# Optimization experiments

Hardware: AMD Instinct MI355X
Metric: run time of the kernel (lower is better)

## Reference

```python
import jax, jax.numpy as jnp
import numpy as np

N, E, F, NC, G = 50000, 400000, 128, 10, 64
EPS_BN = 1e-5
NEG_SLOPE = 0.2


def gat_conv(x, src, dst, W, a_src, a_dst, b, H, C):
    # PyG GATConv (concat=True): h = xW reshaped [N,H,C]; edge score =
    # leaky_relu(a_src.h_j + a_dst.h_i); softmax over incoming edges of i;
    # out_i = sum_j alpha_ij * h_j, then bias.
    n = x.shape[0]
    h = (x @ W).reshape(n, H, C)
    s_src = jnp.sum(h * a_src, axis=-1)  # [N,H]
    s_dst = jnp.sum(h * a_dst, axis=-1)  # [N,H]
    e = jax.nn.leaky_relu(s_src[src] + s_dst[dst], NEG_SLOPE)  # [E',H]
    m = jax.ops.segment_max(e, dst, num_segments=n)
    e = jnp.exp(e - m[dst])
    z = jax.ops.segment_sum(e, dst, num_segments=n)
    alpha = e / (z[dst] + 1e-16)
    msg = h[src] * alpha[:, :, None]  # [E',H,C]
    out = jax.ops.segment_sum(msg, dst, num_segments=n)
    return out.reshape(n, H * C) + b


def batch_norm(x, g, b):
    mu = jnp.mean(x, axis=0)
    var = jnp.var(x, axis=0)
    return g * (x - mu) * jax.lax.rsqrt(var + EPS_BN) + b


def setup_inputs() -> dict:
    key = jax.random.key(0)
    ks = jax.random.split(key, 32)
    d = {}
    d["x"] = jax.random.normal(ks[0], (N, F), dtype=jnp.float32)
    d["edge_index"] = jax.random.randint(ks[1], (2, E), 0, N, dtype=jnp.int32)
    d["batch"] = jnp.sort(jax.random.randint(ks[2], (N,), 0, G, dtype=jnp.int32))

    def nrm(k, shape, scale=0.1):
        return jax.random.normal(k, shape, dtype=jnp.float32) * scale

    # GATConv1: F -> 16, heads=20
    d["W1"] = nrm(ks[3], (F, 20 * 16))
    d["as1"] = nrm(ks[4], (20, 16))
    d["ad1"] = nrm(ks[5], (20, 16))
    d["b1"] = jnp.zeros((320,), jnp.float32)
    d["g1"], d["be1"] = jnp.ones((320,), jnp.float32), jnp.zeros((320,), jnp.float32)
    d["lw1"], d["lb1"] = nrm(ks[6], (320, 16)), jnp.zeros((16,), jnp.float32)
    d["gl1"], d["bel1"] = jnp.ones((16,), jnp.float32), jnp.zeros((16,), jnp.float32)
    # GATConv2: 16 -> 32, heads=16
    d["W2"] = nrm(ks[7], (16, 16 * 32))
    d["as2"] = nrm(ks[8], (16, 32))
    d["ad2"] = nrm(ks[9], (16, 32))
    d["b2"] = jnp.zeros((512,), jnp.float32)
    d["g2"], d["be2"] = jnp.ones((512,), jnp.float32), jnp.zeros((512,), jnp.float32)
    d["lw2"], d["lb2"] = nrm(ks[10], (512, 32)), jnp.zeros((32,), jnp.float32)
    d["gl2"], d["bel2"] = jnp.ones((32,), jnp.float32), jnp.zeros((32,), jnp.float32)
    # GATConv3: 32 -> 48, heads=8
    d["W3"] = nrm(ks[11], (32, 8 * 48))
    d["as3"] = nrm(ks[12], (8, 48))
    d["ad3"] = nrm(ks[13], (8, 48))
    d["b3"] = jnp.zeros((384,), jnp.float32)
    d["g3"], d["be3"] = jnp.ones((384,), jnp.float32), jnp.zeros((384,), jnp.float32)
    d["lwf"], d["lbf"] = nrm(ks[14], (384, NC)), jnp.zeros((NC,), jnp.float32)
    return d


def reference(x, edge_index, batch, W1, as1, ad1, b1, g1, be1, lw1, lb1, gl1, bel1,
              W2, as2, ad2, b2, g2, be2, lw2, lb2, gl2, bel2,
              W3, as3, ad3, b3, g3, be3, lwf, lbf):
    n = x.shape[0]
    loops = jnp.arange(n, dtype=edge_index.dtype)
    src = jnp.concatenate([edge_index[0], loops])
    dst = jnp.concatenate([edge_index[1], loops])

    h = gat_conv(x, src, dst, W1, as1, ad1, b1, 20, 16)
    h = jax.nn.relu(batch_norm(h, g1, be1))
    h = h @ lw1 + lb1
    h = jax.nn.relu(batch_norm(h, gl1, bel1))

    h = gat_conv(h, src, dst, W2, as2, ad2, b2, 16, 32)
    h = jax.nn.relu(batch_norm(h, g2, be2))
    h = h @ lw2 + lb2
    h = jax.nn.relu(batch_norm(h, gl2, bel2))

    h = gat_conv(h, src, dst, W3, as3, ad3, b3, 8, 48)
    h = jax.nn.relu(batch_norm(h, g3, be3))

    # global_mean_pool over graph ids
    sums = jax.ops.segment_sum(h, batch, num_segments=G)
    cnts = jax.ops.segment_sum(jnp.ones((n,), h.dtype), batch, num_segments=G)
    pooled = sums / jnp.maximum(cnts, 1.0)[:, None]
    # dropout is identity in eval mode
    return pooled @ lwf + lbf
```

## Files before the change

kernel.cpp:

```cpp
#include <hip/hip_runtime.h>
#include <cstdint>
#include <cstddef>

#define N_NODES 50000
#define N_EDGES 400000
#define TOT_E   450000
#define G_GRAPHS 64
#define PB 2048
#define SCAN_B 98

typedef unsigned short u16;
typedef unsigned int u32;
typedef unsigned char u8;
typedef __attribute__((ext_vector_type(8))) short s16x8;
typedef __attribute__((ext_vector_type(4))) float f32x4;
typedef __attribute__((ext_vector_type(2))) float f32x2;

__device__ __forceinline__ float b2f(u16 v) {
    union { u32 u; float f; } x; x.u = ((u32)v) << 16; return x.f;
}
__device__ __forceinline__ float lo2f(u32 u) {
    union { u32 u; float f; } x; x.u = u << 16; return x.f;
}
__device__ __forceinline__ float hi2f(u32 u) {
    union { u32 u; float f; } x; x.u = u & 0xffff0000u; return x.f;
}
__device__ __forceinline__ u16 f2b(float f) {
    union { float f; u32 u; } x; x.f = f;
    u32 r = x.u + 0x7fffu + ((x.u >> 16) & 1u);
    return (u16)(r >> 16);
}
__device__ __forceinline__ u32 pack2(float a, float b) {
    return (u32)f2b(a) | ((u32)f2b(b) << 16);
}

__global__ void k_init_deg(int* __restrict__ deg) {
    int i = blockIdx.x * blockDim.x + threadIdx.x;
    if (i < N_NODES) deg[i] = 1;
}

__global__ void k_hist(const int* __restrict__ ei, int* __restrict__ deg) {
    int e = blockIdx.x * blockDim.x + threadIdx.x;
    if (e < N_EDGES) atomicAdd(&deg[ei[N_EDGES + e]], 1);
}

__global__ void k_scan1(const int* __restrict__ deg, int* __restrict__ rowptr,
                        int* __restrict__ bsum) {
    __shared__ int buf[512];
    int tid = threadIdx.x;
    int i = blockIdx.x * 512 + tid;
    int v = (i < N_NODES) ? deg[i] : 0;
    buf[tid] = v;
    __syncthreads();
    for (int off = 1; off < 512; off <<= 1) {
        int t = (tid >= off) ? buf[tid - off] : 0;
        __syncthreads();
        buf[tid] += t;
        __syncthreads();
    }
    if (i < N_NODES) rowptr[i] = buf[tid] - v;
    if (tid == 511) bsum[blockIdx.x] = buf[511];
}

__global__ void k_scan2(int* __restrict__ bsum) {
    __shared__ int buf[128];
    int tid = threadIdx.x;
    int v = (tid < SCAN_B) ? bsum[tid] : 0;
    buf[tid] = v;
    __syncthreads();
    for (int off = 1; off < 128; off <<= 1) {
        int t = (tid >= off) ? buf[tid - off] : 0;
        __syncthreads();
        buf[tid] += t;
        __syncthreads();
    }
    if (tid < SCAN_B) bsum[tid] = buf[tid] - v;
}

__global__ void k_scan3(int* __restrict__ rowptr, int* __restrict__ cursor,
                        const int* __restrict__ bsum) {
    int i = blockIdx.x * blockDim.x + threadIdx.x;
    if (i < N_NODES) {
        int v = rowptr[i] + bsum[i >> 9];
        rowptr[i] = v;
        cursor[i] = v;
    }
    if (i == 0) rowptr[N_NODES] = TOT_E;
}

__global__ void k_scatter(const int* __restrict__ ei, int* __restrict__ cursor,
                          int* __restrict__ col, int* __restrict__ cdst) {
    int e = blockIdx.x * blockDim.x + threadIdx.x;
    if (e < N_EDGES) {
        int s = ei[e], d = ei[N_EDGES + e];
        int p = atomicAdd(&cursor[d], 1);
        col[p] = s;
        cdst[p] = d;
    } else if (e < TOT_E) {
        int i = e - N_EDGES;
        int p = atomicAdd(&cursor[i], 1);
        col[p] = i;
        cdst[p] = i;
    }
}

template<int K, int NO>
__global__ void k_wpack(const float* __restrict__ W, u16* __restrict__ Bp) {
    constexpr int KC = (K + 31) / 32;
    constexpr int NT = NO / 16;
    int idx = blockIdx.x * 256 + threadIdx.x;
    if (idx >= KC * NT * 64) return;
    int lane = idx & 63;
    int t = (idx >> 6) % NT;
    int c = (idx >> 6) / NT;
    int n = t * 16 + (lane & 15);
    int kbase = c * 32 + (lane >> 4) * 8;
    u16 v[8];
#pragma unroll
    for (int j = 0; j < 8; j++) {
        int k = kbase + j;
        v[j] = (k < K) ? f2b(W[(size_t)k * NO + n]) : (u16)0;
    }
    *(uint4*)(Bp + (size_t)idx * 8) = *(const uint4*)v;
}

template<int K, int NO, int H, int C>
__global__ void k_wtilde(const float* __restrict__ W, const float* __restrict__ as,
                         const float* __restrict__ ad, float* __restrict__ wts,
                         float* __restrict__ wtd) {
    static_assert((C % 4) == 0, "C divisible by 4");
    int t = threadIdx.x;
    if (t >= K * H) return;
    int k = t / H, h = t - k * H;
    float s1a = 0.f, s1b = 0.f, s1c = 0.f, s1d = 0.f;
    float s2a = 0.f, s2b = 0.f, s2c = 0.f, s2d = 0.f;
    const float* wr = W + (size_t)k * NO + h * C;
    const float* ar = as + h * C;
    const float* dr = ad + h * C;
    for (int c = 0; c < C; c += 4) {
        float w0 = wr[c], w1 = wr[c + 1], w2 = wr[c + 2], w3 = wr[c + 3];
        s1a = fmaf(w0, ar[c], s1a);     s1b = fmaf(w1, ar[c + 1], s1b);
        s1c = fmaf(w2, ar[c + 2], s1c); s1d = fmaf(w3, ar[c + 3], s1d);
        s2a = fmaf(w0, dr[c], s2a);     s2b = fmaf(w1, dr[c + 1], s2b);
        s2c = fmaf(w2, dr[c + 2], s2c); s2d = fmaf(w3, dr[c + 3], s2d);
    }
    wts[h * K + k] = (s1a + s1b) + (s1c + s1d);
    wtd[h * K + k] = (s2a + s2b) + (s2c + s2d);
}

template<int K>
__global__ void k_xform(const u16* __restrict__ X, const float* __restrict__ sc,
                        const float* __restrict__ sh, u16* __restrict__ Xt) {
    constexpr int NO2 = K / 2;
    int t = blockIdx.x * blockDim.x + threadIdx.x;
    if (t >= N_NODES * NO2) return;
    int w = t % NO2;
    u32 u = ((const u32*)X)[t];
    float2 scv = *(const float2*)&sc[2 * w];
    float2 shv = *(const float2*)&sh[2 * w];
    float a = fmaxf(lo2f(u) * scv.x + shv.x, 0.f);
    float b = fmaxf(hi2f(u) * scv.y + shv.y, 0.f);
    ((u32*)Xt)[t] = pack2(a, b);
}

template<int K, int H>
__global__ void k_scores_x(const u16* __restrict__ Xt, const float* __restrict__ wts,
                           const float* __restrict__ wtd, float* __restrict__ ssrc,
                           float* __restrict__ sdst) {
    int t = blockIdx.x * blockDim.x + threadIdx.x;
    if (t >= N_NODES * H) return;
    int i = t / H, h = t - i * H;
    const uint4* r = (const uint4*)(Xt + (size_t)i * K);
    const float4* ws = (const float4*)(wts + h * K);
    const float4* wd = (const float4*)(wtd + h * K);
    float s1 = 0.f, s2 = 0.f;
#pragma unroll
    for (int c8 = 0; c8 < K / 8; c8++) {
        uint4 u = r[c8];
        float v0 = lo2f(u.x), v1 = hi2f(u.x), v2 = lo2f(u.y), v3 = hi2f(u.y);
        float v4 = lo2f(u.z), v5 = hi2f(u.z), v6 = lo2f(u.w), v7 = hi2f(u.w);
        float4 aa = ws[c8 * 2], ab = ws[c8 * 2 + 1];
        float4 da = wd[c8 * 2], db = wd[c8 * 2 + 1];
        s1 = fmaf(v0, aa.x, fmaf(v1, aa.y, fmaf(v2, aa.z, fmaf(v3, aa.w, s1))));
        s1 = fmaf(v4, ab.x, fmaf(v5, ab.y, fmaf(v6, ab.z, fmaf(v7, ab.w, s1))));
        s2 = fmaf(v0, da.x, fmaf(v1, da.y, fmaf(v2, da.z, fmaf(v3, da.w, s2))));
        s2 = fmaf(v4, db.x, fmaf(v5, db.y, fmaf(v6, db.z, fmaf(v7, db.w, s2))));
    }
    ssrc[t] = s1;
    sdst[t] = s2;
}

template<int H, int K>
__global__ void k_aggx(const u16* __restrict__ Xt, const float* __restrict__ ssrc,
                       const float* __restrict__ sdst, const int* __restrict__ rowptr,
                       const int* __restrict__ col, u16* __restrict__ M) {
    constexpr int WPR = K / 2;
    constexpr int EPR = 64 / WPR;
    constexpr int Q = K / 4;
    static_assert(H * K == 256, "m row must be 256 elems (4/lane)");
    int wid = (int)((blockIdx.x * blockDim.x + threadIdx.x) >> 6);
    int lane = threadIdx.x & 63;
    if (wid >= N_NODES) return;
    int hl = lane / Q;
    int q = lane % Q;
    int lslot = lane / WPR;
    int lword = lane % WPR;
    float sd = (lane < H) ? sdst[(size_t)wid * H + lane] : 0.f;
    f32x2 acc01 = {0.f, 0.f}, acc23 = {0.f, 0.f};
    float z = 0.f;
    int beg = rowptr[wid], end = rowptr[wid + 1];
    for (int base = beg; base < end; base += 64) {
        int nmax = min(64, end - base);
        int myc = (base + lane < end) ? col[base + lane] : 0;
        int j = 0;
        for (; j + EPR <= nmax; j += EPR) {
            int ce = __shfl(myc, j + lslot);
            u32 g = *(const u32*)(Xt + (size_t)ce * K + lword * 2);
            int se[EPR];
#pragma unroll
            for (int e = 0; e < EPR; e++) se[e] = __shfl(myc, j + e);
            float w[EPR];
#pragma unroll
            for (int e = 0; e < EPR; e++) w[e] = 0.f;
            if (lane < H) {
#pragma unroll
                for (int e = 0; e < EPR; e++) {
                    float v = ssrc[(size_t)se[e] * H + lane] + sd;
                    v = (v > 0.f) ? v : 0.2f * v;
                    w[e] = __expf(v);
                    z += w[e];
                }
            }
#pragma unroll
            for (int e = 0; e < EPR; e++) {
                float al = __shfl(w[e], hl);
                u32 xa = __shfl(g, e * WPR + 2 * q);
                u32 xb = __shfl(g, e * WPR + 2 * q + 1);
                f32x2 al2 = {al, al};
                f32x2 xa2 = {lo2f(xa), hi2f(xa)};
                f32x2 xb2 = {lo2f(xb), hi2f(xb)};
                acc01 += xa2 * al2;
                acc23 += xb2 * al2;
            }
        }
        for (; j < nmax; j++) {
            int se = __shfl(myc, j);
            u32 g = *(const u32*)(Xt + (size_t)se * K + lword * 2);
            float w0 = 0.f;
            if (lane < H) {
                float v = ssrc[(size_t)se * H + lane] + sd;
                v = (v > 0.f) ? v : 0.2f * v;
                w0 = __expf(v);
                z += w0;
            }
            float al = __shfl(w0, hl);
            u32 xa = __shfl(g, 2 * q);
            u32 xb = __shfl(g, 2 * q + 1);
            f32x2 al2 = {al, al};
            f32x2 xa2 = {lo2f(xa), hi2f(xa)};
            f32x2 xb2 = {lo2f(xb), hi2f(xb)};
            acc01 += xa2 * al2;
            acc23 += xb2 * al2;
        }
    }
    float zk = __shfl(z, hl);
    float inv = 1.0f / (zk + 1e-16f);
    uint2 o;
    o.x = pack2(acc01.x * inv, acc01.y * inv);
    o.y = pack2(acc23.x * inv, acc23.y * inv);
    u32* orow = (u32*)(M + (size_t)wid * (H * K));
    *(uint2*)&orow[hl * WPR + 2 * q] = o;
}

template<int K, int NO, int C>
__global__ __launch_bounds__(256, 2)
void k_gemmd(const u16* __restrict__ M, const u16* __restrict__ Bp,
             const float* __restrict__ wb, u16* __restrict__ Y,
             float* __restrict__ pst) {
    constexpr int NT = NO / 16;
    constexpr int HK = (NO / C) * K;
    __shared__ float ls[2 * NO];
    int tid = threadIdx.x;
    for (int i = tid; i < 2 * NO; i += 256) ls[i] = 0.f;
    __syncthreads();
    int lane = threadIdx.x & 63;
    int wv = __builtin_amdgcn_readfirstlane((int)(threadIdx.x >> 6));
    int rbase = blockIdx.x * 64 + wv * 16;
    int m = lane & 15, quad = lane >> 4;
    int arow = rbase + m;
    if (arow >= N_NODES) arow = N_NODES - 1;
    const u16* xr = M + (size_t)arow * HK;
#pragma unroll
    for (int t = 0; t < NT; t++) {
        int h = (t * 16) / C;
        s16x8 a;
        if (K == 32 || quad < 2) {
            a = *(const s16x8*)(xr + h * K + quad * 8);
        } else {
#pragma unroll
            for (int j = 0; j < 8; j++) a[j] = 0;
        }
        s16x8 b = *(const s16x8*)(Bp + ((size_t)(t * 64 + lane)) * 8);
        f32x4 acc = (f32x4){0.f, 0.f, 0.f, 0.f};
        acc = __builtin_amdgcn_mfma_f32_16x16x32_bf16(a, b, acc, 0, 0, 0);
        int colb = t * 16 + m;
        float bv = wb[colb];
        float s = 0.f, q = 0.f;
#pragma unroll
        for (int i = 0; i < 4; i++) {
            int grow = rbase + quad * 4 + i;
            float v = acc[i] + bv;
            if (grow < N_NODES) {
                Y[(size_t)grow * NO + colb] = f2b(v);
                s += v;
                q += v * v;
            }
        }
        s += __shfl_xor(s, 16); s += __shfl_xor(s, 32);
        q += __shfl_xor(q, 16); q += __shfl_xor(q, 32);
        if (quad == 0) {
            atomicAdd(&ls[colb], s);
            atomicAdd(&ls[NO + colb], q);
        }
    }
    __syncthreads();
    for (int i = tid; i < 2 * NO; i += 256) atomicAdd(&pst[i], ls[i]);
}

__global__ void k_bnfinal2(const float* __restrict__ pst, const float* __restrict__ g,
                           const float* __restrict__ be, float* __restrict__ scale,
                           float* __restrict__ shift, int NO) {
    int t = threadIdx.x;
    if (t >= NO) return;
    float mu = pst[t] / (float)N_NODES;
    float var = pst[NO + t] / (float)N_NODES - mu * mu;
    float sc = g[t] * rsqrtf(var + 1e-5f);
    scale[t] = sc;
    shift[t] = be[t] - mu * sc;
}

template<int K, int NO, bool XFORM>
__global__ __launch_bounds__(256, 2)
void k_gemm(const float* __restrict__ X, const u16* __restrict__ Bp,
            const float* __restrict__ scale, const float* __restrict__ shift,
            u16* __restrict__ Y) {
    constexpr int KC = (K + 31) / 32;
    constexpr int NT = NO / 16;
    int lane = threadIdx.x & 63;
    int wv = __builtin_amdgcn_readfirstlane((int)(threadIdx.x >> 6));
    int rbase = blockIdx.x * 64 + wv * 16;
    int m = lane & 15, quad = lane >> 4;
    int arow = rbase + m;
    if (arow >= N_NODES) arow = N_NODES - 1;
    const float* xr = X + (size_t)arow * K;

    f32x4 acc[NT];
#pragma unroll
    for (int t = 0; t < NT; t++) acc[t] = (f32x4){0.f, 0.f, 0.f, 0.f};

    for (int c = 0; c < KC; c++) {
        int kbase = c * 32 + quad * 8;
        float xv[8];
        if (kbase < K) {
            float4 va = *(const float4*)&xr[kbase];
            float4 vb = *(const float4*)&xr[kbase + 4];
            xv[0] = va.x; xv[1] = va.y; xv[2] = va.z; xv[3] = va.w;
            xv[4] = vb.x; xv[5] = vb.y; xv[6] = vb.z; xv[7] = vb.w;
            if (XFORM) {
                float4 sa = *(const float4*)&scale[kbase];
                float4 sb = *(const float4*)&scale[kbase + 4];
                float4 ha = *(const float4*)&shift[kbase];
                float4 hb = *(const float4*)&shift[kbase + 4];
                xv[0] = fmaxf(xv[0] * sa.x + ha.x, 0.f);
                xv[1] = fmaxf(xv[1] * sa.y + ha.y, 0.f);
                xv[2] = fmaxf(xv[2] * sa.z + ha.z, 0.f);
                xv[3] = fmaxf(xv[3] * sa.w + ha.w, 0.f);
                xv[4] = fmaxf(xv[4] * sb.x + hb.x, 0.f);
                xv[5] = fmaxf(xv[5] * sb.y + hb.y, 0.f);
                xv[6] = fmaxf(xv[6] * sb.z + hb.z, 0.f);
                xv[7] = fmaxf(xv[7] * sb.w + hb.w, 0.f);
            }
        } else {
#pragma unroll
            for (int j = 0; j < 8; j++) xv[j] = 0.f;
        }
        s16x8 a;
#pragma unroll
        for (int j = 0; j < 8; j++) a[j] = (short)f2b(xv[j]);

        const u16* bp = Bp + (size_t)(c * NT) * 64 * 8;
#pragma unroll
        for (int t = 0; t < NT; t++) {
            s16x8 b = *(const s16x8*)(bp + ((size_t)(t * 64 + lane)) * 8);
            acc[t] = __builtin_amdgcn_mfma_f32_16x16x32_bf16(a, b, acc[t], 0, 0, 0);
        }
    }

#pragma unroll
    for (int t = 0; t < NT; t++) {
        int colb = t * 16 + m;
#pragma unroll
        for (int i = 0; i < 4; i++) {
            int grow = rbase + quad * 4 + i;
            if (grow < N_NODES) Y[(size_t)grow * NO + colb] = f2b(acc[t][i]);
        }
    }
}

template<int K, int NO, bool XFORM, bool BIAS>
__global__ __launch_bounds__(256, 2)
void k_gemmb(const u16* __restrict__ X, const u16* __restrict__ Bp,
             const float* __restrict__ scale, const float* __restrict__ shift,
             const float* __restrict__ wb, u16* __restrict__ Y) {
    constexpr int KC = (K + 31) / 32;
    constexpr int NT = NO / 16;
    int lane = threadIdx.x & 63;
    int wv = __builtin_amdgcn_readfirstlane((int)(threadIdx.x >> 6));
    int rbase = blockIdx.x * 64 + wv * 16;
    int m = lane & 15, quad = lane >> 4;
    int arow = rbase + m;
    if (arow >= N_NODES) arow = N_NODES - 1;
    const u32* xr = (const u32*)(X + (size_t)arow * K);

    f32x4 acc[NT];
#pragma unroll
    for (int t = 0; t < NT; t++) acc[t] = (f32x4){0.f, 0.f, 0.f, 0.f};

    for (int c = 0; c < KC; c++) {
        int kbase = c * 32 + quad * 8;
        s16x8 a;
        if (kbase < K) {
            uint4 w = *(const uint4*)&xr[kbase >> 1];
            if (XFORM) {
                float xv[8];
                xv[0] = lo2f(w.x); xv[1] = hi2f(w.x);
                xv[2] = lo2f(w.y); xv[3] = hi2f(w.y);
                xv[4] = lo2f(w.z); xv[5] = hi2f(w.z);
                xv[6] = lo2f(w.w); xv[7] = hi2f(w.w);
                float4 sa = *(const float4*)&scale[kbase];
                float4 sb = *(const float4*)&scale[kbase + 4];
                float4 ha = *(const float4*)&shift[kbase];
                float4 hb = *(const float4*)&shift[kbase + 4];
                xv[0] = fmaxf(xv[0] * sa.x + ha.x, 0.f);
                xv[1] = fmaxf(xv[1] * sa.y + ha.y, 0.f);
                xv[2] = fmaxf(xv[2] * sa.z + ha.z, 0.f);
                xv[3] = fmaxf(xv[3] * sa.w + ha.w, 0.f);
                xv[4] = fmaxf(xv[4] * sb.x + hb.x, 0.f);
                xv[5] = fmaxf(xv[5] * sb.y + hb.y, 0.f);
                xv[6] = fmaxf(xv[6] * sb.z + hb.z, 0.f);
                xv[7] = fmaxf(xv[7] * sb.w + hb.w, 0.f);
#pragma unroll
                for (int j = 0; j < 8; j++) a[j] = (short)f2b(xv[j]);
            } else {
                a = *(const s16x8*)&w;
            }
        } else {
#pragma unroll
            for (int j = 0; j < 8; j++) a[j] = 0;
        }

        const u16* bp = Bp + (size_t)(c * NT) * 64 * 8;
#pragma unroll
        for (int t = 0; t < NT; t++) {
            s16x8 b = *(const s16x8*)(bp + ((size_t)(t * 64 + lane)) * 8);
            acc[t] = __builtin_amdgcn_mfma_f32_16x16x32_bf16(a, b, acc[t], 0, 0, 0);
        }
    }

#pragma unroll
    for (int t = 0; t < NT; t++) {
        int colb = t * 16 + m;
        float bv = BIAS ? wb[colb] : 0.f;
#pragma unroll
        for (int i = 0; i < 4; i++) {
            int grow = rbase + quad * 4 + i;
            if (grow < N_NODES) Y[(size_t)grow * NO + colb] = f2b(acc[t][i] + bv);
        }
    }
}

template<int H, int C>
__global__ void k_scores(const u16* __restrict__ Hm, const float* __restrict__ asrc,
                         const float* __restrict__ adst, float* __restrict__ ssrc,
                         float* __restrict__ sdst, u8* __restrict__ H8) {
    static_assert(C == 16, "fp8 emit assumes C==16");
    int t = blockIdx.x * blockDim.x + threadIdx.x;
    if (t >= N_NODES * H) return;
    int i = t / H, h = t - i * H;
    const uint4* row4 = (const uint4*)(Hm + (size_t)i * H * C + h * C);
    const float4* a4 = (const float4*)(asrc + h * C);
    const float4* d4 = (const float4*)(adst + h * C);
    float s1 = 0.f, s2 = 0.f;
    uint4 q8;
    u32* qw = (u32*)&q8;
#pragma unroll
    for (int c8 = 0; c8 < C / 8; c8++) {
        uint4 u = row4[c8];
        float v0 = lo2f(u.x), v1 = hi2f(u.x), v2 = lo2f(u.y), v3 = hi2f(u.y);
        float v4 = lo2f(u.z), v5 = hi2f(u.z), v6 = lo2f(u.w), v7 = hi2f(u.w);
        float4 aa = a4[c8 * 2], ab = a4[c8 * 2 + 1];
        float4 da = d4[c8 * 2], db = d4[c8 * 2 + 1];
        s1 = fmaf(v0, aa.x, fmaf(v1, aa.y, fmaf(v2, aa.z, fmaf(v3, aa.w, s1))));
        s1 = fmaf(v4, ab.x, fmaf(v5, ab.y, fmaf(v6, ab.z, fmaf(v7, ab.w, s1))));
        s2 = fmaf(v0, da.x, fmaf(v1, da.y, fmaf(v2, da.z, fmaf(v3, da.w, s2))));
        s2 = fmaf(v4, db.x, fmaf(v5, db.y, fmaf(v6, db.z, fmaf(v7, db.w, s2))));
        u32 qa = 0, qb = 0;
        qa = __builtin_amdgcn_cvt_pk_fp8_f32(v0, v1, qa, false);
        qa = __builtin_amdgcn_cvt_pk_fp8_f32(v2, v3, qa, true);
        qb = __builtin_amdgcn_cvt_pk_fp8_f32(v4, v5, qb, false);
        qb = __builtin_amdgcn_cvt_pk_fp8_f32(v6, v7, qb, true);
        qw[c8 * 2] = qa;
        qw[c8 * 2 + 1] = qb;
    }
    ssrc[t] = s1;
    sdst[t] = s2;
    *(uint4*)(H8 + (size_t)i * (H * C) + h * C) = q8;
}

template<int H, int C>
__global__ void k_agg8(const u8* __restrict__ Hm8, const float* __restrict__ ssrc,
                       const float* __restrict__ sdst, const int* __restrict__ rowptr,
                       const int* __restrict__ col, const float* __restrict__ bias,
                       u16* __restrict__ out) {
    constexpr int HC = H * C;
    constexpr int W2 = HC / 8;
    static_assert(W2 <= 64, "row must fit 64 uint2");
    static_assert((C % 8) == 0, "8-col block must stay within one head");
    int wid = (int)((blockIdx.x * blockDim.x + threadIdx.x) >> 6);
    int lane = threadIdx.x & 63;
    if (wid >= N_NODES) return;
    int hl = (8 * lane) / C;
    int gidx = (lane < W2) ? lane : 0;
    float sd = (lane < H) ? sdst[(size_t)wid * H + lane] : 0.f;
    f32x2 acc01 = {0.f, 0.f}, acc23 = {0.f, 0.f};
    f32x2 acc45 = {0.f, 0.f}, acc67 = {0.f, 0.f};
    float z = 0.f;
    int beg = rowptr[wid], end = rowptr[wid + 1];
#define ACC8(gg, wk) { \
        f32x2 wv_ = {wk, wk}; \
        acc01 += __builtin_amdgcn_cvt_pk_f32_fp8(gg.x, false) * wv_; \
        acc23 += __builtin_amdgcn_cvt_pk_f32_fp8(gg.x, true) * wv_; \
        acc45 += __builtin_amdgcn_cvt_pk_f32_fp8(gg.y, false) * wv_; \
        acc67 += __builtin_amdgcn_cvt_pk_f32_fp8(gg.y, true) * wv_; }
    for (int base = beg; base < end; base += 64) {
        int nmax = min(64, end - base);
        int myc = (base + lane < end) ? col[base + lane] : 0;
        int j = 0;
        for (; j + 4 <= nmax; j += 4) {
            int s0 = __shfl(myc, j), s1 = __shfl(myc, j + 1);
            int s2 = __shfl(myc, j + 2), s3 = __shfl(myc, j + 3);
            uint2 g0 = ((const uint2*)(Hm8 + (size_t)s0 * HC))[gidx];
            uint2 g1 = ((const uint2*)(Hm8 + (size_t)s1 * HC))[gidx];
            uint2 g2 = ((const uint2*)(Hm8 + (size_t)s2 * HC))[gidx];
            uint2 g3 = ((const uint2*)(Hm8 + (size_t)s3 * HC))[gidx];
            float w0 = 0.f, w1 = 0.f, w2 = 0.f, w3 = 0.f;
            if (lane < H) {
                float v0 = ssrc[(size_t)s0 * H + lane] + sd;
                float v1 = ssrc[(size_t)s1 * H + lane] + sd;
                float v2 = ssrc[(size_t)s2 * H + lane] + sd;
                float v3 = ssrc[(size_t)s3 * H + lane] + sd;
                v0 = (v0 > 0.f) ? v0 : 0.2f * v0;
                v1 = (v1 > 0.f) ? v1 : 0.2f * v1;
                v2 = (v2 > 0.f) ? v2 : 0.2f * v2;
                v3 = (v3 > 0.f) ? v3 : 0.2f * v3;
                w0 = __expf(v0); w1 = __expf(v1);
                w2 = __expf(v2); w3 = __expf(v3);
                z += (w0 + w1) + (w2 + w3);
            }
            float wk0 = __shfl(w0, hl), wk1 = __shfl(w1, hl);
            float wk2 = __shfl(w2, hl), wk3 = __shfl(w3, hl);
            ACC8(g0, wk0)
            ACC8(g1, wk1)
            ACC8(g2, wk2)
            ACC8(g3, wk3)
        }
        for (; j < nmax; j++) {
            int s0 = __shfl(myc, j);
            uint2 g0 = ((const uint2*)(Hm8 + (size_t)s0 * HC))[gidx];
            float w0 = 0.f;
            if (lane < H) {
                float v = ssrc[(size_t)s0 * H + lane] + sd;
                v = (v > 0.f) ? v : 0.2f * v;
                w0 = __expf(v);
                z += w0;
            }
            float wk0 = __shfl(w0, hl);
            ACC8(g0, wk0)
        }
    }
#undef ACC8
    float zk = __shfl(z, hl);
    if (lane < W2) {
        float inv = 1.0f / (zk + 1e-16f);
        const float4* b4 = (const float4*)(bias + 8 * lane);
        float4 ba = b4[0], bb = b4[1];
        uint4 o;
        o.x = pack2(fmaf(acc01.x, inv, ba.x), fmaf(acc01.y, inv, ba.y));
        o.y = pack2(fmaf(acc23.x, inv, ba.z), fmaf(acc23.y, inv, ba.w));
        o.z = pack2(fmaf(acc45.x, inv, bb.x), fmaf(acc45.y, inv, bb.y));
        o.w = pack2(fmaf(acc67.x, inv, bb.z), fmaf(acc67.y, inv, bb.w));
        ((uint4*)(out + (size_t)wid * HC))[lane] = o;
    }
}

template<int NO>
__global__ void k_bnstats(const u16* __restrict__ X, float* __restrict__ psum,
                          float* __restrict__ psumsq) {
    constexpr int NO2 = NO / 2;
    constexpr int RPS = (NO2 >= 256) ? 1 : ((255 + NO2) / NO2);
    constexpr int BS = NO2 * RPS;
    __shared__ float2 ls[BS], ls2[BS];
    int c2 = threadIdx.x % NO2;
    int rsub = threadIdx.x / NO2;
    constexpr int chunk = (N_NODES + PB - 1) / PB;
    int r0 = blockIdx.x * chunk;
    int r1 = min(N_NODES, r0 + chunk);
    float2 s = make_float2(0.f, 0.f), s2 = make_float2(0.f, 0.f);
    const u32* Xw = (const u32*)X;
#pragma unroll 4
    for (int r = r0 + rsub; r < r1; r += RPS) {
        u32 u = Xw[(size_t)r * NO2 + c2];
        float a = lo2f(u), b = hi2f(u);
        s.x += a; s.y += b;
        s2.x += a * a; s2.y += b * b;
    }
    if (RPS > 1) {
        ls[threadIdx.x] = s;
        ls2[threadIdx.x] = s2;
        __syncthreads();
        for (int off = BS / 2; off >= NO2; off >>= 1) {
            if (threadIdx.x < off) {
                ls[threadIdx.x].x += ls[threadIdx.x + off].x;
                ls[threadIdx.x].y += ls[threadIdx.x + off].y;
                ls2[threadIdx.x].x += ls2[threadIdx.x + off].x;
                ls2[threadIdx.x].y += ls2[threadIdx.x + off].y;
            }
            __syncthreads();
        }
        s = ls[threadIdx.x];
        s2 = ls2[threadIdx.x];
    }
    if (rsub == 0) {
        *(float2*)&psum[(size_t)blockIdx.x * NO + 2 * c2] = s;
        *(float2*)&psumsq[(size_t)blockIdx.x * NO + 2 * c2] = s2;
    }
}

__global__ void k_bnfinal(const float* __restrict__ psum, const float* __restrict__ psumsq,
                          const float* __restrict__ g, const float* __restrict__ be,
                          float* __restrict__ scale, float* __restrict__ shift, int NO) {
    __shared__ float s1[256], s2[256];
    int col = blockIdx.x;
    int tid = threadIdx.x;
    float a = 0.f, b = 0.f;
    for (int bk = tid; bk < PB; bk += 256) {
        a += psum[(size_t)bk * NO + col];
        b += psumsq[(size_t)bk * NO + col];
    }
    s1[tid] = a;
    s2[tid] = b;
    __syncthreads();
    for (int off = 128; off > 0; off >>= 1) {
        if (tid < off) {
            s1[tid] += s1[tid + off];
            s2[tid] += s2[tid + off];
        }
        __syncthreads();
    }
    if (tid == 0) {
        float mu = s1[0] / (float)N_NODES;
        float var = s2[0] / (float)N_NODES - mu * mu;
        float sc = g[col] * rsqrtf(var + 1e-5f);
        scale[col] = sc;
        shift[col] = be[col] - mu * sc;
    }
}

__global__ void k_bhist(const int* __restrict__ batch, int* __restrict__ cnt) {
    __shared__ int h[G_GRAPHS];
    int tid = threadIdx.x;
    if (tid < G_GRAPHS) h[tid] = 0;
    __syncthreads();
    int i = blockIdx.x * blockDim.x + tid;
    if (i < N_NODES) atomicAdd(&h[batch[i]], 1);
    __syncthreads();
    if (tid < G_GRAPHS) atomicAdd(&cnt[tid], h[tid]);
}

__global__ void k_pool(const u16* __restrict__ X, const int* __restrict__ batch,
                       const float* __restrict__ sc, const float* __restrict__ sh,
                       float* __restrict__ pooled) {
    int t2 = threadIdx.x;
    const int chunk = (N_NODES + gridDim.x - 1) / gridDim.x;
    int r0 = blockIdx.x * chunk;
    int r1 = min(N_NODES, r0 + chunk);
    if (r0 >= N_NODES) return;
    float2 scv = *(const float2*)&sc[2 * t2];
    float2 shv = *(const float2*)&sh[2 * t2];
    const u32* Xw = (const u32*)X;
    float2 acc = make_float2(0.f, 0.f);
    int cur = batch[r0];
    for (int r = r0; r < r1; r++) {
        int gid = batch[r];
        if (gid != cur) {
            atomicAdd(&pooled[(size_t)cur * 384 + 2 * t2], acc.x);
            atomicAdd(&pooled[(size_t)cur * 384 + 2 * t2 + 1], acc.y);
            acc = make_float2(0.f, 0.f);
            cur = gid;
        }
        u32 u = Xw[(size_t)r * 192 + t2];
        acc.x += fmaxf(lo2f(u) * scv.x + shv.x, 0.f);
        acc.y += fmaxf(hi2f(u) * scv.y + shv.y, 0.f);
    }
    atomicAdd(&pooled[(size_t)cur * 384 + 2 * t2], acc.x);
    atomicAdd(&pooled[(size_t)cur * 384 + 2 * t2 + 1], acc.y);
}

__global__ void k_final(const float* __restrict__ pooled, const int* __restrict__ cnt,
                        const float* __restrict__ lwf, const float* __restrict__ lbf,
                        float* __restrict__ out) {
    int wid = (int)((blockIdx.x * blockDim.x + threadIdx.x) >> 6);
    int lane = threadIdx.x & 63;
    if (wid >= G_GRAPHS * 10) return;
    int g = wid / 10, c = wid - g * 10;
    float inv = 1.0f / fmaxf((float)cnt[g], 1.0f);
    float acc = 0.f;
    for (int k = lane; k < 384; k += 64)
        acc += pooled[(size_t)g * 384 + k] * lwf[k * 10 + c];
#pragma unroll
    for (int off = 32; off > 0; off >>= 1) acc += __shfl_xor(acc, off);
    if (lane == 0) out[wid] = acc * inv + lbf[c];
}

extern "C" void kernel_launch(void* const* d_in, const int* in_sizes, int n_in,
                              void* d_out, int out_size, void* d_ws, size_t ws_size,
                              hipStream_t stream) {
    const float* x    = (const float*)d_in[0];
    const int*   ei   = (const int*)d_in[1];
    const int*   batch= (const int*)d_in[2];
    const float* W1   = (const float*)d_in[3];
    const float* as1  = (const float*)d_in[4];
    const float* ad1  = (const float*)d_in[5];
    const float* b1   = (const float*)d_in[6];
    const float* g1   = (const float*)d_in[7];
    const float* be1  = (const float*)d_in[8];
    const float* lw1  = (const float*)d_in[9];
    const float* lb1  = (const float*)d_in[10];
    const float* gl1  = (const float*)d_in[11];
    const float* bel1 = (const float*)d_in[12];
    const float* W2   = (const float*)d_in[13];
    const float* as2  = (const float*)d_in[14];
    const float* ad2  = (const float*)d_in[15];
    const float* b2   = (const float*)d_in[16];
    const float* g2   = (const float*)d_in[17];
    const float* be2  = (const float*)d_in[18];
    const float* lw2  = (const float*)d_in[19];
    const float* lb2  = (const float*)d_in[20];
    const float* gl2  = (const float*)d_in[21];
    const float* bel2 = (const float*)d_in[22];
    const float* W3   = (const float*)d_in[23];
    const float* as3  = (const float*)d_in[24];
    const float* ad3  = (const float*)d_in[25];
    const float* b3   = (const float*)d_in[26];
    const float* g3   = (const float*)d_in[27];
    const float* be3  = (const float*)d_in[28];
    const float* lwf  = (const float*)d_in[29];
    const float* lbf  = (const float*)d_in[30];
    float* out = (float*)d_out;

    char* p = (char*)d_ws;
    auto alloc = [&](size_t bytes) {
        char* r = p;
        p += (bytes + 255) & ~(size_t)255;
        return r;
    };
    int*   rowptr = (int*)alloc(4 * (size_t)(N_NODES + 1));
    int*   cursor = (int*)alloc(4 * (size_t)N_NODES);
    int*   deg    = (int*)alloc(4 * (size_t)N_NODES);
    int*   bsum   = (int*)alloc(4 * (size_t)(SCAN_B + 1));
    int*   col    = (int*)alloc(4 * (size_t)TOT_E);
    int*   cdst   = (int*)alloc(4 * (size_t)TOT_E);
    float* ssrc   = (float*)alloc(4 * (size_t)N_NODES * 20);
    float* sdst   = (float*)alloc(4 * (size_t)N_NODES * 20);
    u16*   hbuf   = (u16*)alloc(2 * (size_t)N_NODES * 512);
    u16*   obuf   = (u16*)alloc(2 * (size_t)N_NODES * 512);
    u16*   xbuf   = (u16*)alloc(2 * (size_t)N_NODES * 32);
    u16*   xtil   = (u16*)alloc(2 * (size_t)N_NODES * 32);
    u8*    hbuf8  = (u8*)alloc((size_t)N_NODES * 320);
    float* psum   = (float*)alloc(4 * (size_t)PB * 512);
    float* psumsq = (float*)alloc(4 * (size_t)PB * 512);
    float* scA    = (float*)alloc(4 * 512);
    float* shA    = (float*)alloc(4 * 512);
    float* scB    = (float*)alloc(4 * 64);
    float* shB    = (float*)alloc(4 * 64);
    float* wts    = (float*)alloc(4 * 256);
    float* wtd    = (float*)alloc(4 * 256);
    float* pstat  = (float*)alloc(4 * 1792);
    float* pst512 = pstat;
    float* pst384 = pstat + 1024;
    float* pooled = (float*)alloc(4 * (size_t)G_GRAPHS * 384);
    int*   cnt    = (int*)alloc(4 * G_GRAPHS);
    u16*   bp1    = (u16*)alloc(2 * (size_t)4 * 20 * 64 * 8);
    u16*   bp2    = (u16*)alloc(2 * (size_t)1 * 32 * 64 * 8);
    u16*   bp3    = (u16*)alloc(2 * (size_t)1 * 24 * 64 * 8);
    u16*   bpl1   = (u16*)alloc(2 * (size_t)10 * 1 * 64 * 8);
    u16*   bpl2   = (u16*)alloc(2 * (size_t)16 * 2 * 64 * 8);
    u16*   mbuf   = hbuf;

    const int LB = (N_NODES + 63) / 64;

    k_init_deg<<<(N_NODES + 255) / 256, 256, 0, stream>>>(deg);
    k_hist<<<(N_EDGES + 255) / 256, 256, 0, stream>>>(ei, deg);
    k_scan1<<<SCAN_B, 512, 0, stream>>>(deg, rowptr, bsum);
    k_scan2<<<1, 128, 0, stream>>>(bsum);
    k_scan3<<<(N_NODES + 255) / 256, 256, 0, stream>>>(rowptr, cursor, bsum);
    k_scatter<<<(TOT_E + 255) / 256, 256, 0, stream>>>(ei, cursor, col, cdst);
    k_wpack<128, 320><<<20, 256, 0, stream>>>(W1, bp1);
    k_wpack<16, 512><<<8, 256, 0, stream>>>(W2, bp2);
    k_wpack<32, 384><<<6, 256, 0, stream>>>(W3, bp3);
    k_wpack<320, 16><<<3, 256, 0, stream>>>(lw1, bpl1);
    k_wpack<512, 32><<<8, 256, 0, stream>>>(lw2, bpl2);
    hipMemsetAsync(pooled, 0, 4 * (size_t)G_GRAPHS * 384 + 256, stream);
    hipMemsetAsync(pstat, 0, 4 * 1792, stream);

    k_gemm<128, 320, false><<<LB, 256, 0, stream>>>(x, bp1, nullptr, nullptr, hbuf);
    k_scores<20, 16><<<(N_NODES * 20 + 255) / 256, 256, 0, stream>>>(hbuf, as1, ad1, ssrc, sdst, hbuf8);
    k_agg8<20, 16><<<(N_NODES + 3) / 4, 256, 0, stream>>>(hbuf8, ssrc, sdst, rowptr, col, b1, obuf);
    k_bnstats<320><<<PB, 320, 0, stream>>>(obuf, psum, psumsq);
    k_bnfinal<<<320, 256, 0, stream>>>(psum, psumsq, g1, be1, scA, shA, 320);
    k_gemmb<320, 16, true, true><<<LB, 256, 0, stream>>>(obuf, bpl1, scA, shA, lb1, xbuf);
    k_bnstats<16><<<PB, 256, 0, stream>>>(xbuf, psum, psumsq);
    k_bnfinal<<<16, 256, 0, stream>>>(psum, psumsq, gl1, bel1, scB, shB, 16);

    k_wtilde<16, 512, 16, 32><<<1, 256, 0, stream>>>(W2, as2, ad2, wts, wtd);
    k_xform<16><<<(N_NODES * 8 + 255) / 256, 256, 0, stream>>>(xbuf, scB, shB, xtil);
    k_scores_x<16, 16><<<(N_NODES * 16 + 255) / 256, 256, 0, stream>>>(xtil, wts, wtd, ssrc, sdst);
    k_aggx<16, 16><<<(N_NODES + 3) / 4, 256, 0, stream>>>(xtil, ssrc, sdst, rowptr, col, mbuf);
    k_gemmd<16, 512, 32><<<LB, 256, 0, stream>>>(mbuf, bp2, b2, obuf, pst512);
    k_bnfinal2<<<1, 512, 0, stream>>>(pst512, g2, be2, scA, shA, 512);
    k_gemmb<512, 32, true, true><<<LB, 256, 0, stream>>>(obuf, bpl2, scA, shA, lb2, xbuf);
    k_bnstats<32><<<PB, 256, 0, stream>>>(xbuf, psum, psumsq);
    k_bnfinal<<<32, 256, 0, stream>>>(psum, psumsq, gl2, bel2, scB, shB, 32);

    k_wtilde<32, 384, 8, 48><<<1, 256, 0, stream>>>(W3, as3, ad3, wts, wtd);
    k_xform<32><<<(N_NODES * 16 + 255) / 256, 256, 0, stream>>>(xbuf, scB, shB, xtil);
    k_scores_x<32, 8><<<(N_NODES * 8 + 255) / 256, 256, 0, stream>>>(xtil, wts, wtd, ssrc, sdst);
    k_aggx<8, 32><<<(N_NODES + 3) / 4, 256, 0, stream>>>(xtil, ssrc, sdst, rowptr, col, mbuf);
    k_gemmd<32, 384, 48><<<LB, 256, 0, stream>>>(mbuf, bp3, b3, obuf, pst384);
    k_bnfinal2<<<1, 512, 0, stream>>>(pst384, g3, be3, scA, shA, 384);

    k_bhist<<<(N_NODES + 255) / 256, 256, 0, stream>>>(batch, cnt);
    k_pool<<<2048, 192, 0, stream>>>(obuf, batch, scA, shA, pooled);
    k_final<<<160, 256, 0, stream>>>(pooled, cnt, lwf, lbf, out);
}
```

Measured before the change: 558.7 us.

## Transpose MFMA operands for vectorized row stores; move BN stats out of gemmd

Swaps the A/B operands of the bf16 MFMA in the GEMM kernels so each lane holds four consecutive output columns of one row, which allows one packed 8-byte store per tile instead of four scattered 2-byte stores. The fused batch-norm statistics (shared-memory and global atomics) are removed from k_gemmd. They are replaced by separate k_bnstats and k_bnfinal launches that re-read the 512- and 384-wide outputs. This trades atomic contention and strided stores for an extra full pass over large intermediate tensors.

```diff
diff --git a/kernel.cpp b/kernel.cpp
--- a/kernel.cpp
+++ b/kernel.cpp
@@ -275,21 +275,19 @@
 template<int K, int NO, int C>
 __global__ __launch_bounds__(256, 2)
 void k_gemmd(const u16* __restrict__ M, const u16* __restrict__ Bp,
-             const float* __restrict__ wb, u16* __restrict__ Y,
-             float* __restrict__ pst) {
+             const float* __restrict__ wb, u16* __restrict__ Y) {
     constexpr int NT = NO / 16;
     constexpr int HK = (NO / C) * K;
-    __shared__ float ls[2 * NO];
-    int tid = threadIdx.x;
-    for (int i = tid; i < 2 * NO; i += 256) ls[i] = 0.f;
-    __syncthreads();
     int lane = threadIdx.x & 63;
     int wv = __builtin_amdgcn_readfirstlane((int)(threadIdx.x >> 6));
     int rbase = blockIdx.x * 64 + wv * 16;
     int m = lane & 15, quad = lane >> 4;
     int arow = rbase + m;
-    if (arow >= N_NODES) arow = N_NODES - 1;
+    bool rowok = arow < N_NODES;
+    if (!rowok) arow = N_NODES - 1;
     const u16* xr = M + (size_t)arow * HK;
+
+    f32x4 acc[NT];
 #pragma unroll
     for (int t = 0; t < NT; t++) {
         int h = (t * 16) / C;
@@ -301,42 +299,21 @@
             for (int j = 0; j < 8; j++) a[j] = 0;
         }
         s16x8 b = *(const s16x8*)(Bp + ((size_t)(t * 64 + lane)) * 8);
-        f32x4 acc = (f32x4){0.f, 0.f, 0.f, 0.f};
-        acc = __builtin_amdgcn_mfma_f32_16x16x32_bf16(a, b, acc, 0, 0, 0);
-        int colb = t * 16 + m;
-        float bv = wb[colb];
-        float s = 0.f, q = 0.f;
-#pragma unroll
-        for (int i = 0; i < 4; i++) {
-            int grow = rbase + quad * 4 + i;
-            float v = acc[i] + bv;
-            if (grow < N_NODES) {
-                Y[(size_t)grow * NO + colb] = f2b(v);
-                s += v;
-                q += v * v;
-            }
-        }
-        s += __shfl_xor(s, 16); s += __shfl_xor(s, 32);
-        q += __shfl_xor(q, 16); q += __shfl_xor(q, 32);
-        if (quad == 0) {
-            atomicAdd(&ls[colb], s);
-            atomicAdd(&ls[NO + colb], q);
-        }
-    }
-    __syncthreads();
-    for (int i = tid; i < 2 * NO; i += 256) atomicAdd(&pst[i], ls[i]);
-}
-
-__global__ void k_bnfinal2(const float* __restrict__ pst, const float* __restrict__ g,
-                           const float* __restrict__ be, float* __restrict__ scale,
-                           float* __restrict__ shift, int NO) {
-    int t = threadIdx.x;
-    if (t >= NO) return;
-    float mu = pst[t] / (float)N_NODES;
-    float var = pst[NO + t] / (float)N_NODES - mu * mu;
-    float sc = g[t] * rsqrtf(var + 1e-5f);
-    scale[t] = sc;
-    shift[t] = be[t] - mu * sc;
+        f32x4 z4 = (f32x4){0.f, 0.f, 0.f, 0.f};
+        acc[t] = __builtin_amdgcn_mfma_f32_16x16x32_bf16(b, a, z4, 0, 0, 0);
+    }
+
+#pragma unroll
+    for (int t = 0; t < NT; t++) {
+        int colb = t * 16 + quad * 4;
+        float4 bv = *(const float4*)&wb[colb];
+        if (rowok) {
+            uint2 o;
+            o.x = pack2(acc[t][0] + bv.x, acc[t][1] + bv.y);
+            o.y = pack2(acc[t][2] + bv.z, acc[t][3] + bv.w);
+            *(uint2*)(Y + (size_t)arow * NO + colb) = o;
+        }
+    }
 }
 
 template<int K, int NO, bool XFORM>
@@ -351,7 +328,8 @@
     int rbase = blockIdx.x * 64 + wv * 16;
     int m = lane & 15, quad = lane >> 4;
     int arow = rbase + m;
-    if (arow >= N_NODES) arow = N_NODES - 1;
+    bool rowok = arow < N_NODES;
+    if (!rowok) arow = N_NODES - 1;
     const float* xr = X + (size_t)arow * K;
 
     f32x4 acc[NT];
@@ -392,17 +370,18 @@
 #pragma unroll
         for (int t = 0; t < NT; t++) {
             s16x8 b = *(const s16x8*)(bp + ((size_t)(t * 64 + lane)) * 8);
-            acc[t] = __builtin_amdgcn_mfma_f32_16x16x32_bf16(a, b, acc[t], 0, 0, 0);
+            acc[t] = __builtin_amdgcn_mfma_f32_16x16x32_bf16(b, a, acc[t], 0, 0, 0);
         }
     }
 
 #pragma unroll
     for (int t = 0; t < NT; t++) {
-        int colb = t * 16 + m;
-#pragma unroll
-        for (int i = 0; i < 4; i++) {
-            int grow = rbase + quad * 4 + i;
-            if (grow < N_NODES) Y[(size_t)grow * NO + colb] = f2b(acc[t][i]);
+        int colb = t * 16 + quad * 4;
+        if (rowok) {
+            uint2 o;
+            o.x = pack2(acc[t][0], acc[t][1]);
+            o.y = pack2(acc[t][2], acc[t][3]);
+            *(uint2*)(Y + (size_t)arow * NO + colb) = o;
         }
     }
 }
@@ -419,7 +398,8 @@
     int rbase = blockIdx.x * 64 + wv * 16;
     int m = lane & 15, quad = lane >> 4;
     int arow = rbase + m;
-    if (arow >= N_NODES) arow = N_NODES - 1;
+    bool rowok = arow < N_NODES;
+    if (!rowok) arow = N_NODES - 1;
     const u32* xr = (const u32*)(X + (size_t)arow * K);
 
     f32x4 acc[NT];
@@ -463,18 +443,20 @@
 #pragma unroll
         for (int t = 0; t < NT; t++) {
             s16x8 b = *(const s16x8*)(bp + ((size_t)(t * 64 + lane)) * 8);
-            acc[t] = __builtin_amdgcn_mfma_f32_16x16x32_bf16(a, b, acc[t], 0, 0, 0);
+            acc[t] = __builtin_amdgcn_mfma_f32_16x16x32_bf16(b, a, acc[t], 0, 0, 0);
         }
     }
 
 #pragma unroll
     for (int t = 0; t < NT; t++) {
-        int colb = t * 16 + m;
-        float bv = BIAS ? wb[colb] : 0.f;
-#pragma unroll
-        for (int i = 0; i < 4; i++) {
-            int grow = rbase + quad * 4 + i;
-            if (grow < N_NODES) Y[(size_t)grow * NO + colb] = f2b(acc[t][i] + bv);
+        int colb = t * 16 + quad * 4;
+        float4 bv = BIAS ? *(const float4*)&wb[colb]
+                         : make_float4(0.f, 0.f, 0.f, 0.f);
+        if (rowok) {
+            uint2 o;
+            o.x = pack2(acc[t][0] + bv.x, acc[t][1] + bv.y);
+            o.y = pack2(acc[t][2] + bv.z, acc[t][3] + bv.w);
+            *(uint2*)(Y + (size_t)arow * NO + colb) = o;
         }
     }
 }
@@ -795,9 +777,6 @@
     float* shB    = (float*)alloc(4 * 64);
     float* wts    = (float*)alloc(4 * 256);
     float* wtd    = (float*)alloc(4 * 256);
-    float* pstat  = (float*)alloc(4 * 1792);
-    float* pst512 = pstat;
-    float* pst384 = pstat + 1024;
     float* pooled = (float*)alloc(4 * (size_t)G_GRAPHS * 384);
     int*   cnt    = (int*)alloc(4 * G_GRAPHS);
     u16*   bp1    = (u16*)alloc(2 * (size_t)4 * 20 * 64 * 8);
@@ -821,7 +800,6 @@
     k_wpack<320, 16><<<3, 256, 0, stream>>>(lw1, bpl1);
     k_wpack<512, 32><<<8, 256, 0, stream>>>(lw2, bpl2);
     hipMemsetAsync(pooled, 0, 4 * (size_t)G_GRAPHS * 384 + 256, stream);
-    hipMemsetAsync(pstat, 0, 4 * 1792, stream);
 
     k_gemm<128, 320, false><<<LB, 256, 0, stream>>>(x, bp1, nullptr, nullptr, hbuf);
     k_scores<20, 16><<<(N_NODES * 20 + 255) / 256, 256, 0, stream>>>(hbuf, as1, ad1, ssrc, sdst, hbuf8);
@@ -836,8 +814,9 @@
     k_xform<16><<<(N_NODES * 8 + 255) / 256, 256, 0, stream>>>(xbuf, scB, shB, xtil);
     k_scores_x<16, 16><<<(N_NODES * 16 + 255) / 256, 256, 0, stream>>>(xtil, wts, wtd, ssrc, sdst);
     k_aggx<16, 16><<<(N_NODES + 3) / 4, 256, 0, stream>>>(xtil, ssrc, sdst, rowptr, col, mbuf);
-    k_gemmd<16, 512, 32><<<LB, 256, 0, stream>>>(mbuf, bp2, b2, obuf, pst512);
-    k_bnfinal2<<<1, 512, 0, stream>>>(pst512, g2, be2, scA, shA, 512);
+    k_gemmd<16, 512, 32><<<LB, 256, 0, stream>>>(mbuf, bp2, b2, obuf);
+    k_bnstats<512><<<PB, 256, 0, stream>>>(obuf, psum, psumsq);
+    k_bnfinal<<<512, 256, 0, stream>>>(psum, psumsq, g2, be2, scA, shA, 512);
     k_gemmb<512, 32, true, true><<<LB, 256, 0, stream>>>(obuf, bpl2, scA, shA, lb2, xbuf);
     k_bnstats<32><<<PB, 256, 0, stream>>>(xbuf, psum, psumsq);
     k_bnfinal<<<32, 256, 0, stream>>>(psum, psumsq, gl2, bel2, scB, shB, 32);
@@ -846,8 +825,9 @@
     k_xform<32><<<(N_NODES * 16 + 255) / 256, 256, 0, stream>>>(xbuf, scB, shB, xtil);
     k_scores_x<32, 8><<<(N_NODES * 8 + 255) / 256, 256, 0, stream>>>(xtil, wts, wtd, ssrc, sdst);
     k_aggx<8, 32><<<(N_NODES + 3) / 4, 256, 0, stream>>>(xtil, ssrc, sdst, rowptr, col, mbuf);
-    k_gemmd<32, 384, 48><<<LB, 256, 0, stream>>>(mbuf, bp3, b3, obuf, pst384);
-    k_bnfinal2<<<1, 512, 0, stream>>>(pst384, g3, be3, scA, shA, 384);
+    k_gemmd<32, 384, 48><<<LB, 256, 0, stream>>>(mbuf, bp3, b3, obuf);
+    k_bnstats<384><<<PB, 384, 0, stream>>>(obuf, psum, psumsq);
+    k_bnfinal<<<384, 256, 0, stream>>>(psum, psumsq, g3, be3, scA, shA, 384);
 
     k_bhist<<<(N_NODES + 255) / 256, 256, 0, stream>>>(batch, cnt);
     k_pool<<<2048, 192, 0, stream>>>(obuf, batch, scA, shA, pooled);
```

Result: no change. 564.6 us (+1.1%).
